# Kernel tuning notes

Measured on AMD Instinct MI355X. Metric: run time of the kernel, lower is better.

## Reference

```python
import jax, jax.numpy as jnp
import numpy as np

DIM = 512          # model dim
DH = 32            # dim_head
WSZ = 8            # window_size
HEADS = DIM // DH  # 16
INNER = HEADS * DH # 512
D4 = DIM // 4      # DPB hidden = 128
EPS = 1e-5


def _ln(x, g, b=None, eps=EPS):
    m = jnp.mean(x, axis=-1, keepdims=True)
    v = jnp.var(x, axis=-1, keepdims=True)
    y = (x - m) * jax.lax.rsqrt(v + eps) * g
    return y if b is None else y + b


def setup_inputs() -> dict:
    key = jax.random.key(0)
    ks = jax.random.split(key, 8)
    g = lambda k, shape, s=0.02: (jax.random.normal(k, shape, jnp.float32) * s)
    return {
        "x": jax.random.normal(ks[0], (16, 64, 64, DIM), jnp.float32),
        "norm_g": jnp.ones((DIM,), jnp.float32),
        "norm_b": jnp.zeros((DIM,), jnp.float32),
        "w_qkv": g(ks[1], (DIM, 3 * INNER)),
        "w_out": g(ks[2], (INNER, DIM)),
        "b_out": jnp.zeros((DIM,), jnp.float32),
        "dpb_w0": g(ks[3], (2, D4)), "dpb_b0": jnp.zeros((D4,), jnp.float32), "dpb_ln0": jnp.ones((D4,), jnp.float32),
        "dpb_w1": g(ks[4], (D4, D4)), "dpb_b1": jnp.zeros((D4,), jnp.float32), "dpb_ln1": jnp.ones((D4,), jnp.float32),
        "dpb_w2": g(ks[5], (D4, D4)), "dpb_b2": jnp.zeros((D4,), jnp.float32), "dpb_ln2": jnp.ones((D4,), jnp.float32),
        "dpb_w3": g(ks[6], (D4, 1)), "dpb_b3": jnp.zeros((1,), jnp.float32),
    }


def reference(x, norm_g, norm_b, w_qkv, w_out, b_out,
              dpb_w0, dpb_b0, dpb_ln0,
              dpb_w1, dpb_b1, dpb_ln1,
              dpb_w2, dpb_b2, dpb_ln2,
              dpb_w3, dpb_b3):
    B, H, W, d = x.shape
    w = WSZ
    scale = DH ** -0.5

    x = _ln(x, norm_g, norm_b)

    # 'short' attention: partition into non-overlapping wxw windows
    # b (h s1) (w s2) d -> (b h w) s1 s2 d
    xw = x.reshape(B, H // w, w, W // w, w, d).transpose(0, 1, 3, 2, 4, 5)
    xw = xw.reshape(-1, w, w, d)  # [nb, w, w, d]

    qkv = xw @ w_qkv  # 1x1 conv == dense, no bias
    q, k, v = jnp.split(qkv, 3, axis=-1)
    to_heads = lambda t: t.reshape(t.shape[0], w * w, HEADS, DH).transpose(0, 2, 1, 3)
    q, k, v = map(to_heads, (q, k, v))  # [nb, h, w*w, dh]

    sim = jnp.einsum('bhid,bhjd->bhij', q * scale, k)  # [nb, h, w*w, w*w]

    # relative-position gather indices (static)
    pos = jnp.arange(w)
    grid = jnp.stack(jnp.meshgrid(pos, pos, indexing='ij'), axis=-1).reshape(-1, 2)
    rel = grid[:, None] - grid[None, :] + (w - 1)
    rel_pos_indices = rel[..., 0] * (2 * w - 1) + rel[..., 1]  # [w*w, w*w]

    # dynamic position bias MLP over the (2w+1)^2 relative offsets
    p = jnp.arange(-w, w + 1)
    rp = jnp.stack(jnp.meshgrid(p, p, indexing='ij'), axis=-1).reshape(-1, 2).astype(jnp.float32)
    h = jax.nn.relu(_ln(rp @ dpb_w0 + dpb_b0, dpb_ln0))
    h = jax.nn.relu(_ln(h @ dpb_w1 + dpb_b1, dpb_ln1))
    h = jax.nn.relu(_ln(h @ dpb_w2 + dpb_b2, dpb_ln2))
    biases = (h @ dpb_w3 + dpb_b3)[:, 0]  # [(2w+1)^2]

    sim = sim + biases[rel_pos_indices]
    attn = jax.nn.softmax(sim, axis=-1)
    out = jnp.einsum('bhij,bhjd->bhid', attn, v)

    out = out.transpose(0, 2, 1, 3).reshape(-1, w, w, INNER)
    out = out @ w_out + b_out  # 1x1 conv with bias

    # (b h w) s1 s2 d -> b (h s1) (w s2) d
    out = out.reshape(B, H // w, W // w, w, w, d).transpose(0, 1, 3, 2, 4, 5)
    return out.reshape(B, H, W, d)
```

## Files before the change

### kernel.cpp

```cpp
#include <hip/hip_runtime.h>
#include <cstdint>
#include <cstddef>

typedef unsigned short u16;
typedef __attribute__((ext_vector_type(8))) short short8;
typedef __attribute__((ext_vector_type(4))) float f32x4;
typedef __attribute__((ext_vector_type(4))) unsigned short us4;

#define AS1 __attribute__((address_space(1)))
#define AS3 __attribute__((address_space(3)))

__device__ __forceinline__ u16 f2bf(float f) {
  union { float f; unsigned u; } v; v.f = f;
  unsigned r = v.u + 0x7fffu + ((v.u >> 16) & 1u);
  return (u16)(r >> 16);
}

__device__ __forceinline__ void gload_lds16(const u16* g, u16* l) {
  __builtin_amdgcn_global_load_lds((AS1 void*)g, (AS3 void*)l, 16, 0, 0);
}

__global__ void ln_cast_kernel(const float* __restrict__ x, const float* __restrict__ g,
                               const float* __restrict__ b, u16* __restrict__ out) {
  const int lane = threadIdx.x & 63;
  const int tok = blockIdx.x * 4 + (threadIdx.x >> 6);
  const float4* row = (const float4*)(x + (size_t)tok * 512);
  float4 v0 = row[lane];
  float4 v1 = row[lane + 64];
  float s = v0.x + v0.y + v0.z + v0.w + v1.x + v1.y + v1.z + v1.w;
  float q = v0.x*v0.x + v0.y*v0.y + v0.z*v0.z + v0.w*v0.w
          + v1.x*v1.x + v1.y*v1.y + v1.z*v1.z + v1.w*v1.w;
#pragma unroll
  for (int m = 1; m < 64; m <<= 1) { s += __shfl_xor(s, m, 64); q += __shfl_xor(q, m, 64); }
  const float mean = s * (1.0f / 512.0f);
  const float var = q * (1.0f / 512.0f) - mean * mean;
  const float r = rsqrtf(var + 1e-5f);
  const float4* g4 = (const float4*)g;
  const float4* b4 = (const float4*)b;
  float4 ga = g4[lane], gb = g4[lane + 64];
  float4 ba = b4[lane], bb = b4[lane + 64];
  us4 o0 = { f2bf((v0.x - mean) * r * ga.x + ba.x), f2bf((v0.y - mean) * r * ga.y + ba.y),
             f2bf((v0.z - mean) * r * ga.z + ba.z), f2bf((v0.w - mean) * r * ga.w + ba.w) };
  us4 o1 = { f2bf((v1.x - mean) * r * gb.x + bb.x), f2bf((v1.y - mean) * r * gb.y + bb.y),
             f2bf((v1.z - mean) * r * gb.z + bb.z), f2bf((v1.w - mean) * r * gb.w + bb.w) };
  *(us4*)(out + (size_t)tok * 512 + lane * 4) = o0;
  *(us4*)(out + (size_t)tok * 512 + 256 + lane * 4) = o1;
}

__global__ void prep_w_kernel(const float* __restrict__ wqkv, const float* __restrict__ wout,
                              u16* __restrict__ wqkvT, u16* __restrict__ woutT) {
  int idx = blockIdx.x * blockDim.x + threadIdx.x;
  if (idx < 512 * 1536) {
    int n = idx >> 9, k = idx & 511;
    wqkvT[idx] = f2bf(wqkv[k * 1536 + n]);
  } else {
    int j = idx - 512 * 1536;
    if (j < 512 * 512) {
      int n = j >> 9, k = j & 511;
      woutT[j] = f2bf(wout[k * 512 + n]);
    }
  }
}

__device__ __forceinline__ float lnrelu128(float a, float g, float* red, int tid) {
  float s = a, q = a * a;
#pragma unroll
  for (int m = 1; m < 64; m <<= 1) { s += __shfl_xor(s, m, 64); q += __shfl_xor(q, m, 64); }
  __syncthreads();
  if ((tid & 63) == 0) { red[tid >> 6] = s; red[2 + (tid >> 6)] = q; }
  __syncthreads();
  float S = red[0] + red[1], Q = red[2] + red[3];
  float mean = S * (1.f / 128.f);
  float var = Q * (1.f / 128.f) - mean * mean;
  float y = (a - mean) * rsqrtf(var + 1e-5f) * g;
  return fmaxf(y, 0.f);
}

__global__ void dpb_mlp_kernel(const float* __restrict__ w0, const float* __restrict__ b0, const float* __restrict__ g0,
                               const float* __restrict__ w1, const float* __restrict__ b1, const float* __restrict__ g1,
                               const float* __restrict__ w2, const float* __restrict__ b2, const float* __restrict__ g2,
                               const float* __restrict__ w3, const float* __restrict__ b3,
                               float* __restrict__ biases) {
  __shared__ float h[128];
  __shared__ float red[4];
  const int tid = threadIdx.x;
  const int row = blockIdx.x;
  const float p0 = (float)(row / 17) - 8.0f;
  const float p1 = (float)(row % 17) - 8.0f;
  float a = p0 * w0[tid] + p1 * w0[128 + tid] + b0[tid];
  a = lnrelu128(a, g0[tid], red, tid);
  h[tid] = a;
  __syncthreads();
  float acc = b1[tid];
  for (int i = 0; i < 128; ++i) acc += h[i] * w1[i * 128 + tid];
  acc = lnrelu128(acc, g1[tid], red, tid);
  h[tid] = acc;
  __syncthreads();
  float acc2 = b2[tid];
  for (int i = 0; i < 128; ++i) acc2 += h[i] * w2[i * 128 + tid];
  acc2 = lnrelu128(acc2, g2[tid], red, tid);
  float t = acc2 * w3[tid];
#pragma unroll
  for (int m = 1; m < 64; m <<= 1) t += __shfl_xor(t, m, 64);
  __syncthreads();
  if ((tid & 63) == 0) red[tid >> 6] = t;
  __syncthreads();
  if (tid == 0) biases[row] = red[0] + red[1] + b3[0];
}

__global__ void dpb_table_kernel(const float* __restrict__ biases, float* __restrict__ table) {
  int t = blockIdx.x * blockDim.x + threadIdx.x;
  if (t < 4096) {
    int i = t >> 6, j = t & 63;
    int r0 = (i >> 3) - (j >> 3) + 7;
    int r1 = (i & 7) - (j & 7) + 7;
    table[t] = biases[r0 * 15 + r1];
  }
}

template <int CT, bool F32OUT>
__global__ __launch_bounds__(512, 2) void gemm256_kernel(const u16* __restrict__ A, const u16* __restrict__ BT,
                                                         void* __restrict__ Cv, const float* __restrict__ bias) {
  __shared__ __align__(16) u16 lds[65536];
  const int tid = threadIdx.x;
  const int w = tid >> 6, l = tid & 63;
  const int wm = w >> 2, wn = w & 3;
  const int cr = l & 15, cg = l >> 4;
  const int pc8 = (cg ^ ((cr + (cr >> 2)) & 3)) * 8;

  const int nwg = gridDim.x;
  const int q = nwg >> 3;
  const int swz = (blockIdx.x & 7) * q + (blockIdx.x >> 3);
  const int rt = swz / CT, ct = swz % CT;
  const size_t brow = (size_t)rt * 256;
  const size_t bcol = (size_t)ct * 256;
  const int N = CT * 256;

  const int srow = tid >> 2;
  const int sch8 = ((tid & 3) ^ ((srow + (srow >> 2)) & 3)) * 8;

  const f32x4 zero = {0.f, 0.f, 0.f, 0.f};
  f32x4 acc[8][4];
#pragma unroll
  for (int i = 0; i < 8; ++i)
#pragma unroll
    for (int j = 0; j < 4; ++j) acc[i][j] = zero;

  const u16* aP = &lds[(wm * 128 + cr) * 32 + pc8];
  const u16* bP = &lds[(wn * 64 + cr) * 32 + pc8];

#define STAGE_HALF(G, GROW0, KCOL, LBASE)                                          \
  do {                                                                             \
    const u16* g0_ = (G) + ((GROW0) + srow) * 512 + (KCOL) + sch8;                 \
    gload_lds16(g0_, &lds[(LBASE) + w * 512]);                                     \
    gload_lds16(g0_ + 128 * 512, &lds[(LBASE) + 4096 + w * 512]);                  \
  } while (0)

  STAGE_HALF(A, brow, 0, 0);
  STAGE_HALF(BT, bcol, 0, 32768);
  STAGE_HALF(A, brow, 32, 8192);
  STAGE_HALF(BT, bcol, 32, 32768 + 8192);
  asm volatile("s_waitcnt vmcnt(4)" ::: "memory");
  __builtin_amdgcn_s_barrier();
  __builtin_amdgcn_sched_barrier(0);

#pragma unroll 2
  for (int kt = 0; kt < 8; ++kt) {
    const int cur = kt & 1;
    const int nbuf = cur ^ 1;
    const int ktn = (kt < 7) ? kt + 1 : 7;
    const int kcn = ktn * 64;
    const int abase = cur * 16384;
    const int bbase = 32768 + cur * 16384;
    short8 af[8], bfr[2];

#pragma unroll
    for (int fr = 0; fr < 8; ++fr) af[fr] = *(const short8*)(aP + abase + fr * 512);
#pragma unroll
    for (int c = 0; c < 2; ++c) bfr[c] = *(const short8*)(bP + bbase + c * 512);
    STAGE_HALF(A, brow, kcn, nbuf * 16384);
    __builtin_amdgcn_s_barrier();
    __builtin_amdgcn_sched_barrier(0);
    __builtin_amdgcn_s_setprio(1);
#pragma unroll
    for (int fr = 0; fr < 8; ++fr) {
      acc[fr][0] = __builtin_amdgcn_mfma_f32_16x16x32_bf16(af[fr], bfr[0], acc[fr][0], 0, 0, 0);
      acc[fr][1] = __builtin_amdgcn_mfma_f32_16x16x32_bf16(af[fr], bfr[1], acc[fr][1], 0, 0, 0);
    }
    __builtin_amdgcn_s_setprio(0);
    __builtin_amdgcn_s_barrier();
    __builtin_amdgcn_sched_barrier(0);

#pragma unroll
    for (int c = 0; c < 2; ++c) bfr[c] = *(const short8*)(bP + bbase + (2 + c) * 512);
    STAGE_HALF(BT, bcol, kcn, 32768 + nbuf * 16384);
    __builtin_amdgcn_s_barrier();
    __builtin_amdgcn_sched_barrier(0);
    __builtin_amdgcn_s_setprio(1);
#pragma unroll
    for (int fr = 0; fr < 8; ++fr) {
      acc[fr][2] = __builtin_amdgcn_mfma_f32_16x16x32_bf16(af[fr], bfr[0], acc[fr][2], 0, 0, 0);
      acc[fr][3] = __builtin_amdgcn_mfma_f32_16x16x32_bf16(af[fr], bfr[1], acc[fr][3], 0, 0, 0);
    }
    __builtin_amdgcn_s_setprio(0);
    asm volatile("s_waitcnt vmcnt(4)" ::: "memory");
    __builtin_amdgcn_s_barrier();
    __builtin_amdgcn_sched_barrier(0);

#pragma unroll
    for (int fr = 0; fr < 8; ++fr) af[fr] = *(const short8*)(aP + abase + 8192 + fr * 512);
#pragma unroll
    for (int c = 0; c < 2; ++c) bfr[c] = *(const short8*)(bP + bbase + 8192 + c * 512);
    STAGE_HALF(A, brow, kcn + 32, nbuf * 16384 + 8192);
    __builtin_amdgcn_s_barrier();
    __builtin_amdgcn_sched_barrier(0);
    __builtin_amdgcn_s_setprio(1);
#pragma unroll
    for (int fr = 0; fr < 8; ++fr) {
      acc[fr][0] = __builtin_amdgcn_mfma_f32_16x16x32_bf16(af[fr], bfr[0], acc[fr][0], 0, 0, 0);
      acc[fr][1] = __builtin_amdgcn_mfma_f32_16x16x32_bf16(af[fr], bfr[1], acc[fr][1], 0, 0, 0);
    }
    __builtin_amdgcn_s_setprio(0);
    __builtin_amdgcn_s_barrier();
    __builtin_amdgcn_sched_barrier(0);

#pragma unroll
    for (int c = 0; c < 2; ++c) bfr[c] = *(const short8*)(bP + bbase + 8192 + (2 + c) * 512);
    STAGE_HALF(BT, bcol, kcn + 32, 32768 + nbuf * 16384 + 8192);
    __builtin_amdgcn_s_barrier();
    __builtin_amdgcn_sched_barrier(0);
    __builtin_amdgcn_s_setprio(1);
#pragma unroll
    for (int fr = 0; fr < 8; ++fr) {
      acc[fr][2] = __builtin_amdgcn_mfma_f32_16x16x32_bf16(af[fr], bfr[0], acc[fr][2], 0, 0, 0);
      acc[fr][3] = __builtin_amdgcn_mfma_f32_16x16x32_bf16(af[fr], bfr[1], acc[fr][3], 0, 0, 0);
    }
    __builtin_amdgcn_s_setprio(0);
    asm volatile("s_waitcnt vmcnt(4)" ::: "memory");
    __builtin_amdgcn_s_barrier();
    __builtin_amdgcn_sched_barrier(0);
  }
#undef STAGE_HALF

  asm volatile("s_waitcnt vmcnt(0)" ::: "memory");
  __builtin_amdgcn_sched_barrier(0);

  if (F32OUT) {
    float* C = (float*)Cv;
#pragma unroll
    for (int fc = 0; fc < 4; ++fc) {
      size_t col = bcol + wn * 64 + fc * 16 + cr;
      float bv = bias[col];
#pragma unroll
      for (int fr = 0; fr < 8; ++fr)
#pragma unroll
        for (int reg = 0; reg < 4; ++reg) {
          size_t r = brow + wm * 128 + fr * 16 + cg * 4 + reg;
          C[r * N + col] = acc[fr][fc][reg] + bv;
        }
    }
  } else {
    u16* C = (u16*)Cv;
#pragma unroll
    for (int fc = 0; fc < 4; ++fc) {
      size_t col = bcol + wn * 64 + fc * 16 + cr;
#pragma unroll
      for (int fr = 0; fr < 8; ++fr)
#pragma unroll
        for (int reg = 0; reg < 4; ++reg) {
          size_t r = brow + wm * 128 + fr * 16 + cg * 4 + reg;
          C[r * N + col] = f2bf(acc[fr][fc][reg]);
        }
    }
  }
}

__global__ __launch_bounds__(64) void attn_kernel(const u16* __restrict__ qkv,
                                                  const float* __restrict__ table,
                                                  u16* __restrict__ aout) {
  __shared__ __align__(16) u16 P[64 * 72];
  __shared__ __align__(16) u16 VT[32 * 72];
  const int l = threadIdx.x;
  const int cr = l & 15, cg = l >> 4;
  const int head = blockIdx.x & 15;
  const int win = blockIdx.x >> 4;
  const int base = ((win >> 6) << 12) + (((win >> 3) & 7) << 9) + ((win & 7) << 3);

  {
    const size_t row = base + ((l >> 3) << 6) + (l & 7);
    const u16* vp = qkv + row * 1536 + 1024 + head * 32;
    short8 v0 = *(const short8*)(vp);
    short8 v1 = *(const short8*)(vp + 8);
    short8 v2 = *(const short8*)(vp + 16);
    short8 v3 = *(const short8*)(vp + 24);
#pragma unroll
    for (int j = 0; j < 8; ++j) {
      VT[j * 72 + l] = (u16)v0[j];
      VT[(8 + j) * 72 + l] = (u16)v1[j];
      VT[(16 + j) * 72 + l] = (u16)v2[j];
      VT[(24 + j) * 72 + l] = (u16)v3[j];
    }
  }

  short8 qf[4], kf[4];
#pragma unroll
  for (int mt = 0; mt < 4; ++mt) {
    int t = mt * 16 + cr;
    size_t row = base + ((t >> 3) << 6) + (t & 7);
    qf[mt] = *(const short8*)(qkv + row * 1536 + head * 32 + cg * 8);
    kf[mt] = *(const short8*)(qkv + row * 1536 + 512 + head * 32 + cg * 8);
  }

  const f32x4 zero = {0.f, 0.f, 0.f, 0.f};
  f32x4 s[4][4];
#pragma unroll
  for (int mt = 0; mt < 4; ++mt)
#pragma unroll
    for (int nt = 0; nt < 4; ++nt)
      s[mt][nt] = __builtin_amdgcn_mfma_f32_16x16x32_bf16(qf[mt], kf[nt], zero, 0, 0, 0);

  const float scale = 0.17677669529663689f;
#pragma unroll
  for (int mt = 0; mt < 4; ++mt) {
#pragma unroll
    for (int reg = 0; reg < 4; ++reg) {
      const int r = mt * 16 + cg * 4 + reg;
      float v[4];
      float mx = -3.0e38f;
#pragma unroll
      for (int nt = 0; nt < 4; ++nt) {
        v[nt] = s[mt][nt][reg] * scale + table[r * 64 + nt * 16 + cr];
        mx = fmaxf(mx, v[nt]);
      }
#pragma unroll
      for (int m2 = 1; m2 < 16; m2 <<= 1) mx = fmaxf(mx, __shfl_xor(mx, m2, 64));
      float sum = 0.f;
#pragma unroll
      for (int nt = 0; nt < 4; ++nt) { v[nt] = __expf(v[nt] - mx); sum += v[nt]; }
#pragma unroll
      for (int m2 = 1; m2 < 16; m2 <<= 1) sum += __shfl_xor(sum, m2, 64);
      float inv = 1.0f / sum;
#pragma unroll
      for (int nt = 0; nt < 4; ++nt) P[r * 72 + nt * 16 + cr] = f2bf(v[nt] * inv);
    }
  }
  __syncthreads();

  f32x4 o[4][2];
#pragma unroll
  for (int mt = 0; mt < 4; ++mt) { o[mt][0] = zero; o[mt][1] = zero; }
#pragma unroll
  for (int kk = 0; kk < 2; ++kk) {
    short8 pf[4], vf[2];
#pragma unroll
    for (int mt = 0; mt < 4; ++mt) pf[mt] = *(const short8*)&P[(mt * 16 + cr) * 72 + kk * 32 + cg * 8];
#pragma unroll
    for (int n2 = 0; n2 < 2; ++n2) vf[n2] = *(const short8*)&VT[(n2 * 16 + cr) * 72 + kk * 32 + cg * 8];
#pragma unroll
    for (int mt = 0; mt < 4; ++mt)
#pragma unroll
      for (int n2 = 0; n2 < 2; ++n2)
        o[mt][n2] = __builtin_amdgcn_mfma_f32_16x16x32_bf16(pf[mt], vf[n2], o[mt][n2], 0, 0, 0);
  }

#pragma unroll
  for (int mt = 0; mt < 4; ++mt)
#pragma unroll
    for (int n2 = 0; n2 < 2; ++n2)
#pragma unroll
      for (int reg = 0; reg < 4; ++reg) {
        int t = mt * 16 + cg * 4 + reg;
        size_t row = base + ((t >> 3) << 6) + (t & 7);
        aout[row * 512 + head * 32 + n2 * 16 + cr] = f2bf(o[mt][n2][reg]);
      }
}

extern "C" void kernel_launch(void* const* d_in, const int* in_sizes, int n_in,
                              void* d_out, int out_size, void* d_ws, size_t ws_size,
                              hipStream_t stream) {
  const float* x = (const float*)d_in[0];
  const float* norm_g = (const float*)d_in[1];
  const float* norm_b = (const float*)d_in[2];
  const float* w_qkv = (const float*)d_in[3];
  const float* w_out = (const float*)d_in[4];
  const float* b_out = (const float*)d_in[5];
  const float* dw0 = (const float*)d_in[6];
  const float* db0 = (const float*)d_in[7];
  const float* dg0 = (const float*)d_in[8];
  const float* dw1 = (const float*)d_in[9];
  const float* db1 = (const float*)d_in[10];
  const float* dg1 = (const float*)d_in[11];
  const float* dw2 = (const float*)d_in[12];
  const float* db2 = (const float*)d_in[13];
  const float* dg2 = (const float*)d_in[14];
  const float* dw3 = (const float*)d_in[15];
  const float* db3 = (const float*)d_in[16];

  char* ws = (char*)d_ws;
  size_t off = 0;
  auto take = [&](size_t bytes) { char* p = ws + off; off += (bytes + 255) & ~(size_t)255; return p; };
  u16* xln = (u16*)take(65536ull * 512 * 2);
  u16* wqkvT = (u16*)take(1536 * 512 * 2);
  u16* woutT = (u16*)take(512 * 512 * 2);
  float* biases = (float*)take(289 * 4);
  float* table = (float*)take(4096 * 4);

  size_t rem = (ws_size > off) ? ws_size - off : 0;
  int nch = 4;
  if (rem >= 65536ull * 2048 * 2 + 512) nch = 1;
  else if (rem >= 32768ull * 2048 * 2 + 512) nch = 2;
  const int rows = 65536 / nch;
  u16* qkvbuf = (u16*)take((size_t)rows * 1536 * 2);
  u16* attnbuf = (u16*)take((size_t)rows * 512 * 2);

  ln_cast_kernel<<<16384, 256, 0, stream>>>(x, norm_g, norm_b, xln);
  prep_w_kernel<<<4096, 256, 0, stream>>>(w_qkv, w_out, wqkvT, woutT);
  dpb_mlp_kernel<<<289, 128, 0, stream>>>(dw0, db0, dg0, dw1, db1, dg1, dw2, db2, dg2, dw3, db3, biases);
  dpb_table_kernel<<<16, 256, 0, stream>>>(biases, table);

  for (int c = 0; c < nch; ++c) {
    const u16* Ac = xln + (size_t)c * rows * 512;
    gemm256_kernel<6, false><<<(rows / 256) * 6, 512, 0, stream>>>(Ac, wqkvT, (void*)qkvbuf, nullptr);
    attn_kernel<<<(rows / 64) * 16, 64, 0, stream>>>(qkvbuf, table, attnbuf);
    float* Cc = (float*)d_out + (size_t)c * rows * 512;
    gemm256_kernel<2, true><<<(rows / 256) * 2, 512, 0, stream>>>(attnbuf, woutT, (void*)Cc, b_out);
  }
}
```

Before: 379.7 us.

## Swap MFMA operands for vectorized epilogue stores and remap tile order

Swapping the A and B operands of the MFMA transposes the accumulator layout. Each lane now holds four consecutive output columns of one row, so the epilogue can write float4 or packed bf16x4 stores instead of scattered scalar stores. The block-to-tile mapping also changes so that groups of 8 consecutive blocks span 8 row tiles sharing a column tile, replacing the previous XCD-style swizzle. This cuts the store instruction count and the number of uncoalesced writes, at the risk of worse L2 locality under the new tile order.

```diff
diff --git a/kernel.cpp b/kernel.cpp
--- a/kernel.cpp
+++ b/kernel.cpp
@@ -128,10 +128,10 @@
   const int cr = l & 15, cg = l >> 4;
   const int pc8 = (cg ^ ((cr + (cr >> 2)) & 3)) * 8;
 
-  const int nwg = gridDim.x;
-  const int q = nwg >> 3;
-  const int swz = (blockIdx.x & 7) * q + (blockIdx.x >> 3);
-  const int rt = swz / CT, ct = swz % CT;
+  const int hw = blockIdx.x;
+  const int ix = hw >> 3;
+  const int rt = (hw & 7) + 8 * (ix / CT);
+  const int ct = ix % CT;
   const size_t brow = (size_t)rt * 256;
   const size_t bcol = (size_t)ct * 256;
   const int N = CT * 256;
@@ -184,8 +184,8 @@
     __builtin_amdgcn_s_setprio(1);
 #pragma unroll
     for (int fr = 0; fr < 8; ++fr) {
-      acc[fr][0] = __builtin_amdgcn_mfma_f32_16x16x32_bf16(af[fr], bfr[0], acc[fr][0], 0, 0, 0);
-      acc[fr][1] = __builtin_amdgcn_mfma_f32_16x16x32_bf16(af[fr], bfr[1], acc[fr][1], 0, 0, 0);
+      acc[fr][0] = __builtin_amdgcn_mfma_f32_16x16x32_bf16(bfr[0], af[fr], acc[fr][0], 0, 0, 0);
+      acc[fr][1] = __builtin_amdgcn_mfma_f32_16x16x32_bf16(bfr[1], af[fr], acc[fr][1], 0, 0, 0);
     }
     __builtin_amdgcn_s_setprio(0);
     __builtin_amdgcn_s_barrier();
@@ -199,8 +199,8 @@
     __builtin_amdgcn_s_setprio(1);
 #pragma unroll
     for (int fr = 0; fr < 8; ++fr) {
-      acc[fr][2] = __builtin_amdgcn_mfma_f32_16x16x32_bf16(af[fr], bfr[0], acc[fr][2], 0, 0, 0);
-      acc[fr][3] = __builtin_amdgcn_mfma_f32_16x16x32_bf16(af[fr], bfr[1], acc[fr][3], 0, 0, 0);
+      acc[fr][2] = __builtin_amdgcn_mfma_f32_16x16x32_bf16(bfr[0], af[fr], acc[fr][2], 0, 0, 0);
+      acc[fr][3] = __builtin_amdgcn_mfma_f32_16x16x32_bf16(bfr[1], af[fr], acc[fr][3], 0, 0, 0);
     }
     __builtin_amdgcn_s_setprio(0);
     asm volatile("s_waitcnt vmcnt(4)" ::: "memory");
@@ -217,8 +217,8 @@
     __builtin_amdgcn_s_setprio(1);
 #pragma unroll
     for (int fr = 0; fr < 8; ++fr) {
-      acc[fr][0] = __builtin_amdgcn_mfma_f32_16x16x32_bf16(af[fr], bfr[0], acc[fr][0], 0, 0, 0);
-      acc[fr][1] = __builtin_amdgcn_mfma_f32_16x16x32_bf16(af[fr], bfr[1], acc[fr][1], 0, 0, 0);
+      acc[fr][0] = __builtin_amdgcn_mfma_f32_16x16x32_bf16(bfr[0], af[fr], acc[fr][0], 0, 0, 0);
+      acc[fr][1] = __builtin_amdgcn_mfma_f32_16x16x32_bf16(bfr[1], af[fr], acc[fr][1], 0, 0, 0);
     }
     __builtin_amdgcn_s_setprio(0);
     __builtin_amdgcn_s_barrier();
@@ -232,8 +232,8 @@
     __builtin_amdgcn_s_setprio(1);
 #pragma unroll
     for (int fr = 0; fr < 8; ++fr) {
-      acc[fr][2] = __builtin_amdgcn_mfma_f32_16x16x32_bf16(af[fr], bfr[0], acc[fr][2], 0, 0, 0);
-      acc[fr][3] = __builtin_amdgcn_mfma_f32_16x16x32_bf16(af[fr], bfr[1], acc[fr][3], 0, 0, 0);
+      acc[fr][2] = __builtin_amdgcn_mfma_f32_16x16x32_bf16(bfr[0], af[fr], acc[fr][2], 0, 0, 0);
+      acc[fr][3] = __builtin_amdgcn_mfma_f32_16x16x32_bf16(bfr[1], af[fr], acc[fr][3], 0, 0, 0);
     }
     __builtin_amdgcn_s_setprio(0);
     asm volatile("s_waitcnt vmcnt(4)" ::: "memory");
@@ -249,28 +249,29 @@
     float* C = (float*)Cv;
 #pragma unroll
     for (int fc = 0; fc < 4; ++fc) {
-      size_t col = bcol + wn * 64 + fc * 16 + cr;
-      float bv = bias[col];
-#pragma unroll
-      for (int fr = 0; fr < 8; ++fr)
-#pragma unroll
-        for (int reg = 0; reg < 4; ++reg) {
-          size_t r = brow + wm * 128 + fr * 16 + cg * 4 + reg;
-          C[r * N + col] = acc[fr][fc][reg] + bv;
-        }
+      size_t col = bcol + wn * 64 + fc * 16 + cg * 4;
+      float4 bv = *(const float4*)&bias[col];
+#pragma unroll
+      for (int fr = 0; fr < 8; ++fr) {
+        size_t r = brow + wm * 128 + fr * 16 + cr;
+        float4 o = { acc[fr][fc][0] + bv.x, acc[fr][fc][1] + bv.y,
+                     acc[fr][fc][2] + bv.z, acc[fr][fc][3] + bv.w };
+        *(float4*)(C + r * N + col) = o;
+      }
     }
   } else {
     u16* C = (u16*)Cv;
 #pragma unroll
     for (int fc = 0; fc < 4; ++fc) {
-      size_t col = bcol + wn * 64 + fc * 16 + cr;
-#pragma unroll
-      for (int fr = 0; fr < 8; ++fr)
-#pragma unroll
-        for (int reg = 0; reg < 4; ++reg) {
-          size_t r = brow + wm * 128 + fr * 16 + cg * 4 + reg;
-          C[r * N + col] = f2bf(acc[fr][fc][reg]);
-        }
+      size_t col = bcol + wn * 64 + fc * 16 + cg * 4;
+#pragma unroll
+      for (int fr = 0; fr < 8; ++fr) {
+        size_t r = brow + wm * 128 + fr * 16 + cr;
+        uint2 p;
+        p.x = (unsigned)f2bf(acc[fr][fc][0]) | ((unsigned)f2bf(acc[fr][fc][1]) << 16);
+        p.y = (unsigned)f2bf(acc[fr][fc][2]) | ((unsigned)f2bf(acc[fr][fc][3]) << 16);
+        *(uint2*)(C + r * N + col) = p;
+      }
     }
   }
 }
```

After: 386.9 us. Within noise of the previous version (+1.9%).
